# Optimization experiments

Hardware: AMD Instinct MI355X
Metric: run time of the kernel (lower is better)

## Reference

```python
import jax, jax.numpy as jnp
import numpy as np

EPS = 1e-5

def _rmsnorm(x, eps=1e-6):
    # non-affine RMSNorm over last dim (BitNet SubLN-style pre-quant norm)
    return x * jax.lax.rsqrt(jnp.mean(x * x, axis=-1, keepdims=True) + eps)

def _act_quant(x):
    # per-token int8 absmax quantization
    scale = 127.0 / jnp.clip(jnp.max(jnp.abs(x), axis=-1, keepdims=True), EPS)
    return jnp.clip(jnp.round(x * scale), -128, 127) / scale

def _weight_quant(w):
    # per-tensor ternary (1.58-bit) quantization
    scale = 1.0 / jnp.clip(jnp.mean(jnp.abs(w)), EPS)
    return jnp.clip(jnp.round(w * scale), -1, 1) / scale

def _ste(a, q):
    # straight-through estimator: forward = q, backward grad flows to a
    return a + jax.lax.stop_gradient(q - a)

def _bitlinear(x, w):
    # x: [..., in_features], w: [out_features, in_features], no bias
    xn = _rmsnorm(x)
    xq = _ste(xn, _act_quant(xn))
    wq = _ste(w, _weight_quant(w))
    return jnp.einsum('bsd,hd->bsh', xq, wq)


def setup_inputs() -> dict:
    key = jax.random.key(0)
    k_x, k1, k2, k3 = jax.random.split(key, 4)
    B, S, D, H = 4, 4096, 2048, 5632  # hidden = 256*ceil(2048*8/3 / 256)
    return {
        'x': jax.random.normal(k_x, (B, S, D), dtype=jnp.float32),
        'w1': jax.random.normal(k1, (H, D), dtype=jnp.float32) * 0.02,
        'w2': jax.random.normal(k2, (H, D), dtype=jnp.float32) * 0.02,
        'w3': jax.random.normal(k3, (D, H), dtype=jnp.float32) * 0.02,
    }


def reference(x, w1, w2, w3):
    gate = jax.nn.silu(_bitlinear(x, w1))
    up = _bitlinear(x, w2)
    return _bitlinear(gate * up, w3)
```

## Files before the change

kernel.cpp:

```cpp
#include <hip/hip_runtime.h>

typedef int i32x4 __attribute__((ext_vector_type(4)));

static constexpr int M_TOK = 16384;
static constexpr int D_IN  = 2048;
static constexpr int H_FF  = 5632;
static constexpr int NW    = H_FF * D_IN;

__device__ __forceinline__ void async16(const void* g, void* l) {
    __builtin_amdgcn_global_load_lds((__attribute__((address_space(1))) void*)g,
                                     (__attribute__((address_space(3))) void*)l,
                                     16, 0, 0);
}

__device__ __forceinline__ void sbar() {
    asm volatile("" ::: "memory");
    __builtin_amdgcn_s_barrier();
    asm volatile("" ::: "memory");
}
__device__ __forceinline__ void wait_lgkm0() {
    asm volatile("s_waitcnt lgkmcnt(0)" ::: "memory");
    __builtin_amdgcn_sched_barrier(0);
}

__global__ void absum_partial(const float4* __restrict__ w, int n4, double* __restrict__ part) {
    __shared__ double s[256];
    const int t = threadIdx.x;
    double acc = 0.0;
    for (int i = blockIdx.x * 256 + t; i < n4; i += gridDim.x * 256) {
        float4 v = w[i];
        acc += fabs((double)v.x) + fabs((double)v.y) + fabs((double)v.z) + fabs((double)v.w);
    }
    s[t] = acc;
    __syncthreads();
    for (int o = 128; o > 0; o >>= 1) {
        if (t < o) s[t] += s[t + o];
        __syncthreads();
    }
    if (t == 0) part[blockIdx.x] = s[0];
}

__global__ void finalize_scales(const double* __restrict__ parts, double* __restrict__ scales,
                                int nblocks, double inv_n) {
    const int t = threadIdx.x;
    if (t < 3) {
        const double* p = parts + t * nblocks;
        double s = 0.0;
        for (int i = 0; i < nblocks; ++i) s += p[i];
        double c = fmax(s * inv_n, 1e-5);
        scales[t * 2]     = 1.0 / c;
        scales[t * 2 + 1] = c;
    }
}

__global__ void quant_w_kernel(const float4* __restrict__ w, unsigned int* __restrict__ tw,
                               const double* __restrict__ scales, int idx, int n4) {
    const double s = scales[idx * 2];
    const int stride = gridDim.x * blockDim.x;
    for (int i = blockIdx.x * blockDim.x + threadIdx.x; i < n4; i += stride) {
        float4 v = w[i];
        int q0 = (int)fmin(fmax(rint((double)v.x * s), -1.0), 1.0);
        int q1 = (int)fmin(fmax(rint((double)v.y * s), -1.0), 1.0);
        int q2 = (int)fmin(fmax(rint((double)v.z * s), -1.0), 1.0);
        int q3 = (int)fmin(fmax(rint((double)v.w * s), -1.0), 1.0);
        tw[i] = (unsigned int)((q0 & 255) | ((q1 & 255) << 8) |
                               ((q2 & 255) << 16) | ((q3 & 255) << 24));
    }
}

__global__ void quant_x_kernel(const float* __restrict__ x, signed char* __restrict__ qx,
                               double* __restrict__ cx) {
    __shared__ double ssum[256];
    __shared__ float  smax[256];
    const int token = blockIdx.x;
    const int t = threadIdx.x;
    const float4* xr = (const float4*)(x + (size_t)token * D_IN);
    float4 v0 = xr[t];
    float4 v1 = xr[t + 256];
    double ss = (double)v0.x*v0.x + (double)v0.y*v0.y + (double)v0.z*v0.z + (double)v0.w*v0.w
              + (double)v1.x*v1.x + (double)v1.y*v1.y + (double)v1.z*v1.z + (double)v1.w*v1.w;
    float mx = fmaxf(fmaxf(fmaxf(fabsf(v0.x), fabsf(v0.y)), fmaxf(fabsf(v0.z), fabsf(v0.w))),
                     fmaxf(fmaxf(fabsf(v1.x), fabsf(v1.y)), fmaxf(fabsf(v1.z), fabsf(v1.w))));
    ssum[t] = ss; smax[t] = mx;
    __syncthreads();
    for (int o = 128; o > 0; o >>= 1) {
        if (t < o) { ssum[t] += ssum[t + o]; smax[t] = fmaxf(smax[t], smax[t + o]); }
        __syncthreads();
    }
    const double ms    = ssum[0] * (1.0 / (double)D_IN);
    const double r     = 1.0 / sqrt(ms + 1e-6);
    const double den   = fmax((double)smax[0] * r, 1e-5);
    const double scale = 127.0 / den;
    if (t == 0) cx[token] = den * (1.0 / 127.0);

    int q0 = (int)fmin(fmax(rint(((double)v0.x * r) * scale), -128.0), 127.0);
    int q1 = (int)fmin(fmax(rint(((double)v0.y * r) * scale), -128.0), 127.0);
    int q2 = (int)fmin(fmax(rint(((double)v0.z * r) * scale), -128.0), 127.0);
    int q3 = (int)fmin(fmax(rint(((double)v0.w * r) * scale), -128.0), 127.0);
    int q4 = (int)fmin(fmax(rint(((double)v1.x * r) * scale), -128.0), 127.0);
    int q5 = (int)fmin(fmax(rint(((double)v1.y * r) * scale), -128.0), 127.0);
    int q6 = (int)fmin(fmax(rint(((double)v1.z * r) * scale), -128.0), 127.0);
    int q7 = (int)fmin(fmax(rint(((double)v1.w * r) * scale), -128.0), 127.0);
    unsigned int* qr = (unsigned int*)(qx + (size_t)token * D_IN);
    qr[t]       = (unsigned int)((q0 & 255) | ((q1 & 255) << 8) | ((q2 & 255) << 16) | ((q3 & 255) << 24));
    qr[t + 256] = (unsigned int)((q4 & 255) | ((q5 & 255) << 8) | ((q6 & 255) << 16) | ((q7 & 255) << 24));
}

__global__ void quant_h_kernel(float* __restrict__ h, double* __restrict__ ch) {
    __shared__ double ssum[256];
    __shared__ float  smax[256];
    const int token = blockIdx.x;
    const int t = threadIdx.x;
    float* hr = h + (size_t)token * H_FF;
    float vals[22];
    double ss = 0.0;
    float mx = 0.f;
#pragma unroll
    for (int k = 0; k < 22; ++k) {
        float v = hr[t + 256 * k];
        vals[k] = v;
        ss += (double)v * (double)v;
        mx = fmaxf(mx, fabsf(v));
    }
    ssum[t] = ss; smax[t] = mx;
    __syncthreads();
    for (int o = 128; o > 0; o >>= 1) {
        if (t < o) { ssum[t] += ssum[t + o]; smax[t] = fmaxf(smax[t], smax[t + o]); }
        __syncthreads();
    }
    const double ms    = ssum[0] * (1.0 / (double)H_FF);
    const double r     = 1.0 / sqrt(ms + 1e-6);
    const double den   = fmax((double)smax[0] * r, 1e-5);
    const double scale = 127.0 / den;
    if (t == 0) ch[token] = den * (1.0 / 127.0);
    signed char* qr = (signed char*)hr;
#pragma unroll
    for (int k = 0; k < 22; ++k) {
        qr[t + 256 * k] =
            (signed char)(int)fmin(fmax(rint(((double)vals[k] * r) * scale), -128.0), 127.0);
    }
}

__global__ void __launch_bounds__(512, 2) gemm12_kernel(
    const signed char* __restrict__ qx,
    const signed char* __restrict__ tw1,
    const signed char* __restrict__ tw2,
    const double* __restrict__ cx,
    const double* __restrict__ scales,
    float* __restrict__ h)
{
    __shared__ __attribute__((aligned(16))) signed char lds[3][32768];

    const int t  = threadIdx.x;
    const int bn = blockIdx.x;
    const int bm = blockIdx.y;

    const int srow = t >> 2;
    const int scol = (t & 3) << 4;
    const signed char* gA  = qx  + (size_t)(bm * 256 + srow) * D_IN + scol;
    const signed char* gB1 = tw1 + (size_t)(bn * 128 + srow) * D_IN + scol;
    const signed char* gB2 = tw2 + (size_t)(bn * 128 + srow) * D_IN + scol;
    const size_t arstep = (size_t)128 * D_IN;
    const int l16 = t * 16;

    const int lane = t & 63;
    const int wv = t >> 6;
    const int wm = wv & 3;
    const int wn = wv >> 2;
    const int lm = lane & 15;
    const int kg = lane >> 4;

    int aoff[4], boff[4];
#pragma unroll
    for (int i = 0; i < 4; ++i) aoff[i] = (wm * 64 + i * 16 + lm) * 64 + kg * 16;
#pragma unroll
    for (int j = 0; j < 4; ++j) boff[j] = (wn * 64 + j * 16 + lm) * 64 + kg * 16;

    const i32x4 izero = {0, 0, 0, 0};
    i32x4 acc1[4][4], acc2[4][4];
#pragma unroll
    for (int i = 0; i < 4; ++i)
#pragma unroll
        for (int j = 0; j < 4; ++j) { acc1[i][j] = izero; acc2[i][j] = izero; }

    constexpr int NT = D_IN / 64;

#define STAGE_A12(buf, kt) { const int go = (kt) * 64;                       \
        async16(gA + go,          &lds[buf][l16]);                           \
        async16(gA + arstep + go, &lds[buf][l16 + 8192]); }
#define STAGE_B12(buf, kt) { const int go = (kt) * 64;                       \
        async16(gB1 + go, &lds[buf][16384 + l16]);                           \
        async16(gB2 + go, &lds[buf][24576 + l16]); }

    STAGE_A12(0, 0); STAGE_B12(0, 0);
    STAGE_A12(1, 1); STAGE_B12(1, 1);
    asm volatile("s_waitcnt vmcnt(4)" ::: "memory");
    sbar();

    for (int kt = 0; kt < NT; ++kt) {
        const int cur = kt % 3;
        const int nxt = (kt + 2) % 3;

        i32x4 a[4], b[4];
#pragma unroll
        for (int i = 0; i < 4; ++i) a[i] = *(const i32x4*)&lds[cur][aoff[i]];
#pragma unroll
        for (int j = 0; j < 4; ++j) b[j] = *(const i32x4*)&lds[cur][16384 + boff[j]];
        if (kt + 2 < NT) STAGE_A12(nxt, kt + 2);
        sbar();
        wait_lgkm0();
        __builtin_amdgcn_s_setprio(1);
#pragma unroll
        for (int i = 0; i < 4; ++i)
#pragma unroll
            for (int j = 0; j < 4; ++j)
                acc1[i][j] = __builtin_amdgcn_mfma_i32_16x16x64_i8(a[i], b[j], acc1[i][j], 0, 0, 0);
        __builtin_amdgcn_s_setprio(0);
        sbar();

#pragma unroll
        for (int j = 0; j < 4; ++j) b[j] = *(const i32x4*)&lds[cur][24576 + boff[j]];
        if (kt + 2 < NT) STAGE_B12(nxt, kt + 2);
        sbar();
        wait_lgkm0();
        __builtin_amdgcn_s_setprio(1);
#pragma unroll
        for (int i = 0; i < 4; ++i)
#pragma unroll
            for (int j = 0; j < 4; ++j)
                acc2[i][j] = __builtin_amdgcn_mfma_i32_16x16x64_i8(a[i], b[j], acc2[i][j], 0, 0, 0);
        __builtin_amdgcn_s_setprio(0);

        if (kt + 2 < NT)      { asm volatile("s_waitcnt vmcnt(4)" ::: "memory"); }
        else if (kt + 1 < NT) { asm volatile("s_waitcnt vmcnt(0)" ::: "memory"); }
        sbar();
    }
#undef STAGE_A12
#undef STAGE_B12

    const double cw1 = scales[1];
    const double cw2 = scales[3];
#pragma unroll
    for (int i = 0; i < 4; ++i) {
#pragma unroll
        for (int v = 0; v < 4; ++v) {
            const int row = bm * 256 + wm * 64 + i * 16 + kg * 4 + v;
            const double c  = cx[row];
            const double s1 = c * cw1, s2 = c * cw2;
            float* hp = h + (size_t)row * H_FF + bn * 128 + wn * 64 + lm;
#pragma unroll
            for (int j = 0; j < 4; ++j) {
                float g  = (float)((double)acc1[i][j][v] * s1);
                float u  = (float)((double)acc2[i][j][v] * s2);
                float sg = g / (1.0f + expf(-g));
                hp[j * 16] = sg * u;
            }
        }
    }
}

__global__ void __launch_bounds__(512, 2) gemm3_kernel(
    const signed char* __restrict__ qh,
    const signed char* __restrict__ tw3,
    const double* __restrict__ ch,
    const double* __restrict__ scales,
    float* __restrict__ out)
{
    __shared__ __attribute__((aligned(16))) signed char lds[3][32768];

    const int t  = threadIdx.x;
    const int bn = blockIdx.x;
    const int bm = blockIdx.y;

    const int srow = t >> 2;
    const int scol = (t & 3) << 4;
    const size_t qh_stride = (size_t)4 * H_FF;
    const signed char* gA = qh  + (size_t)(bm * 256 + srow) * qh_stride + scol;
    const signed char* gB = tw3 + (size_t)(bn * 256 + srow) * H_FF + scol;
    const size_t arstep = (size_t)128 * qh_stride;
    const size_t brstep = (size_t)128 * H_FF;
    const int l16 = t * 16;

    const int lane = t & 63;
    const int wv = t >> 6;
    const int wm = wv >> 2;
    const int wn = wv & 3;
    const int lm = lane & 15;
    const int kg = lane >> 4;

    int aoff[8], boff[4];
#pragma unroll
    for (int i = 0; i < 8; ++i) aoff[i] = (wm * 128 + i * 16 + lm) * 64 + kg * 16;
#pragma unroll
    for (int j = 0; j < 4; ++j) boff[j] = (wn * 64 + j * 16 + lm) * 64 + kg * 16;

    const i32x4 izero = {0, 0, 0, 0};
    i32x4 acc[8][4];
#pragma unroll
    for (int i = 0; i < 8; ++i)
#pragma unroll
        for (int j = 0; j < 4; ++j) acc[i][j] = izero;

    constexpr int NT = H_FF / 64;

#define STAGE_A3(buf, kt) { const int go = (kt) * 64;                        \
        async16(gA + go,          &lds[buf][l16]);                           \
        async16(gA + arstep + go, &lds[buf][l16 + 8192]); }
#define STAGE_B3(buf, kt) { const int go = (kt) * 64;                        \
        async16(gB + go,          &lds[buf][16384 + l16]);                   \
        async16(gB + brstep + go, &lds[buf][24576 + l16]); }

    STAGE_A3(0, 0); STAGE_B3(0, 0);
    STAGE_A3(1, 1); STAGE_B3(1, 1);
    asm volatile("s_waitcnt vmcnt(4)" ::: "memory");
    sbar();

    for (int kt = 0; kt < NT; ++kt) {
        const int cur = kt % 3;
        const int nxt = (kt + 2) % 3;

        i32x4 a[4], b[4], a2[4];
#pragma unroll
        for (int i = 0; i < 4; ++i) a[i] = *(const i32x4*)&lds[cur][aoff[i]];
#pragma unroll
        for (int j = 0; j < 4; ++j) b[j] = *(const i32x4*)&lds[cur][16384 + boff[j]];
        if (kt + 2 < NT) STAGE_A3(nxt, kt + 2);
        sbar();
        wait_lgkm0();
        __builtin_amdgcn_s_setprio(1);
#pragma unroll
        for (int i = 0; i < 4; ++i)
#pragma unroll
            for (int j = 0; j < 4; ++j)
                acc[i][j] = __builtin_amdgcn_mfma_i32_16x16x64_i8(a[i], b[j], acc[i][j], 0, 0, 0);
        __builtin_amdgcn_s_setprio(0);
        sbar();

#pragma unroll
        for (int i = 0; i < 4; ++i) a2[i] = *(const i32x4*)&lds[cur][aoff[i + 4]];
        if (kt + 2 < NT) STAGE_B3(nxt, kt + 2);
        sbar();
        wait_lgkm0();
        __builtin_amdgcn_s_setprio(1);
#pragma unroll
        for (int i = 0; i < 4; ++i)
#pragma unroll
            for (int j = 0; j < 4; ++j)
                acc[i + 4][j] = __builtin_amdgcn_mfma_i32_16x16x64_i8(a2[i], b[j], acc[i + 4][j], 0, 0, 0);
        __builtin_amdgcn_s_setprio(0);

        if (kt + 2 < NT)      { asm volatile("s_waitcnt vmcnt(4)" ::: "memory"); }
        else if (kt + 1 < NT) { asm volatile("s_waitcnt vmcnt(0)" ::: "memory"); }
        sbar();
    }
#undef STAGE_A3
#undef STAGE_B3

    const double cw3 = scales[5];
#pragma unroll
    for (int i = 0; i < 8; ++i) {
#pragma unroll
        for (int v = 0; v < 4; ++v) {
            const int row = bm * 256 + wm * 128 + i * 16 + kg * 4 + v;
            const double sc = ch[row] * cw3;
            float* op = out + (size_t)row * D_IN + bn * 256 + wn * 64 + lm;
#pragma unroll
            for (int j = 0; j < 4; ++j) op[j * 16] = (float)((double)acc[i][j][v] * sc);
        }
    }
}

extern "C" void kernel_launch(void* const* d_in, const int* in_sizes, int n_in,
                              void* d_out, int out_size, void* d_ws, size_t ws_size,
                              hipStream_t stream) {
    const float* x  = (const float*)d_in[0];
    const float* w1 = (const float*)d_in[1];
    const float* w2 = (const float*)d_in[2];
    const float* w3 = (const float*)d_in[3];

    char* ws = (char*)d_ws;
    double*      scales = (double*)(ws + 0);
    double*      parts  = (double*)(ws + 256);
    double*      cx     = (double*)(ws + 25088);
    double*      ch     = (double*)(ws + 156416);
    signed char* tw1    = (signed char*)(ws + 287744);
    signed char* tw2    = (signed char*)(ws + 11822336);
    signed char* tw3    = (signed char*)(ws + 23356928);
    float*       hb     = (float*)(ws + 34891520);
    signed char* qx     = (signed char*)(ws + 403990528);

    absum_partial<<<1024, 256, 0, stream>>>((const float4*)w1, NW / 4, parts);
    absum_partial<<<1024, 256, 0, stream>>>((const float4*)w2, NW / 4, parts + 1024);
    absum_partial<<<1024, 256, 0, stream>>>((const float4*)w3, NW / 4, parts + 2048);
    finalize_scales<<<1, 64, 0, stream>>>(parts, scales, 1024, 1.0 / (double)NW);
    quant_w_kernel<<<2048, 256, 0, stream>>>((const float4*)w1, (unsigned int*)tw1, scales, 0, NW / 4);
    quant_w_kernel<<<2048, 256, 0, stream>>>((const float4*)w2, (unsigned int*)tw2, scales, 1, NW / 4);
    quant_w_kernel<<<2048, 256, 0, stream>>>((const float4*)w3, (unsigned int*)tw3, scales, 2, NW / 4);
    quant_x_kernel<<<M_TOK, 256, 0, stream>>>(x, qx, cx);
    gemm12_kernel<<<dim3(H_FF / 128, M_TOK / 256), 512, 0, stream>>>(qx, tw1, tw2, cx, scales, hb);
    quant_h_kernel<<<M_TOK, 256, 0, stream>>>(hb, ch);
    gemm3_kernel<<<dim3(D_IN / 256, M_TOK / 256), 512, 0, stream>>>((const signed char*)hb,
                                                                    tw3, ch, scales,
                                                                    (float*)d_out);
}
```

Before: 1.114 ms.

## Swizzle LDS layout, remap block order for XCDs, vectorize h quantization

Both int8 GEMMs now XOR-swizzle the 16-byte column chunk when staging tiles into LDS and when reading MFMA fragments, to cut LDS bank conflicts. Both GEMMs also switch to a 1D grid with a remapped block index, so neighbouring blocks that run on the same XCD share A/B tiles in L2. The h quantization kernel now loads float2 and writes packed 16-bit pairs instead of single floats and bytes. The swizzle has to match exactly between the stage writes and the fragment reads, or results will be wrong.

```diff
diff --git a/kernel.cpp b/kernel.cpp
--- a/kernel.cpp
+++ b/kernel.cpp
@@ -112,15 +112,16 @@
     const int token = blockIdx.x;
     const int t = threadIdx.x;
     float* hr = h + (size_t)token * H_FF;
-    float vals[22];
+    const float2* h2 = (const float2*)hr;
+    float2 vals[11];
     double ss = 0.0;
     float mx = 0.f;
 #pragma unroll
-    for (int k = 0; k < 22; ++k) {
-        float v = hr[t + 256 * k];
+    for (int k = 0; k < 11; ++k) {
+        float2 v = h2[t + 256 * k];
         vals[k] = v;
-        ss += (double)v * (double)v;
-        mx = fmaxf(mx, fabsf(v));
+        ss += (double)v.x * (double)v.x + (double)v.y * (double)v.y;
+        mx = fmaxf(mx, fmaxf(fabsf(v.x), fabsf(v.y)));
     }
     ssum[t] = ss; smax[t] = mx;
     __syncthreads();
@@ -133,13 +134,15 @@
     const double den   = fmax((double)smax[0] * r, 1e-5);
     const double scale = 127.0 / den;
     if (t == 0) ch[token] = den * (1.0 / 127.0);
-    signed char* qr = (signed char*)hr;
-#pragma unroll
-    for (int k = 0; k < 22; ++k) {
-        qr[t + 256 * k] =
-            (signed char)(int)fmin(fmax(rint(((double)vals[k] * r) * scale), -128.0), 127.0);
-    }
-}
+    unsigned short* qr = (unsigned short*)hr;
+#pragma unroll
+    for (int k = 0; k < 11; ++k) {
+        int a = (int)fmin(fmax(rint(((double)vals[k].x * r) * scale), -128.0), 127.0);
+        int b = (int)fmin(fmax(rint(((double)vals[k].y * r) * scale), -128.0), 127.0);
+        qr[t + 256 * k] = (unsigned short)((a & 255) | ((b & 255) << 8));
+    }
+}
+
 
 __global__ void __launch_bounds__(512, 2) gemm12_kernel(
     const signed char* __restrict__ qx,
@@ -151,12 +154,13 @@
 {
     __shared__ __attribute__((aligned(16))) signed char lds[3][32768];
 
-    const int t  = threadIdx.x;
-    const int bn = blockIdx.x;
-    const int bm = blockIdx.y;
+    const int t = threadIdx.x;
+    const int swz = (blockIdx.x & 7) * 352 + (blockIdx.x >> 3);
+    const int bm  = swz & 63;
+    const int bn  = swz >> 6;
 
     const int srow = t >> 2;
-    const int scol = (t & 3) << 4;
+    const int scol = (((t & 3) ^ ((t >> 3) & 3)) << 4);
     const signed char* gA  = qx  + (size_t)(bm * 256 + srow) * D_IN + scol;
     const signed char* gB1 = tw1 + (size_t)(bn * 128 + srow) * D_IN + scol;
     const signed char* gB2 = tw2 + (size_t)(bn * 128 + srow) * D_IN + scol;
@@ -169,12 +173,13 @@
     const int wn = wv >> 2;
     const int lm = lane & 15;
     const int kg = lane >> 4;
+    const int koff = ((kg ^ ((lm >> 1) & 3)) << 4);
 
     int aoff[4], boff[4];
 #pragma unroll
-    for (int i = 0; i < 4; ++i) aoff[i] = (wm * 64 + i * 16 + lm) * 64 + kg * 16;
-#pragma unroll
-    for (int j = 0; j < 4; ++j) boff[j] = (wn * 64 + j * 16 + lm) * 64 + kg * 16;
+    for (int i = 0; i < 4; ++i) aoff[i] = (wm * 64 + i * 16 + lm) * 64 + koff;
+#pragma unroll
+    for (int j = 0; j < 4; ++j) boff[j] = (wn * 64 + j * 16 + lm) * 64 + koff;
 
     const i32x4 izero = {0, 0, 0, 0};
     i32x4 acc1[4][4], acc2[4][4];
@@ -268,12 +273,13 @@
 {
     __shared__ __attribute__((aligned(16))) signed char lds[3][32768];
 
-    const int t  = threadIdx.x;
-    const int bn = blockIdx.x;
-    const int bm = blockIdx.y;
+    const int t = threadIdx.x;
+    const int swz = (blockIdx.x & 7) * 64 + (blockIdx.x >> 3);
+    const int bm  = swz & 63;
+    const int bn  = swz >> 6;
 
     const int srow = t >> 2;
-    const int scol = (t & 3) << 4;
+    const int scol = (((t & 3) ^ ((t >> 3) & 3)) << 4);
     const size_t qh_stride = (size_t)4 * H_FF;
     const signed char* gA = qh  + (size_t)(bm * 256 + srow) * qh_stride + scol;
     const signed char* gB = tw3 + (size_t)(bn * 256 + srow) * H_FF + scol;
@@ -287,12 +293,13 @@
     const int wn = wv & 3;
     const int lm = lane & 15;
     const int kg = lane >> 4;
+    const int koff = ((kg ^ ((lm >> 1) & 3)) << 4);
 
     int aoff[8], boff[4];
 #pragma unroll
-    for (int i = 0; i < 8; ++i) aoff[i] = (wm * 128 + i * 16 + lm) * 64 + kg * 16;
-#pragma unroll
-    for (int j = 0; j < 4; ++j) boff[j] = (wn * 64 + j * 16 + lm) * 64 + kg * 16;
+    for (int i = 0; i < 8; ++i) aoff[i] = (wm * 128 + i * 16 + lm) * 64 + koff;
+#pragma unroll
+    for (int j = 0; j < 4; ++j) boff[j] = (wn * 64 + j * 16 + lm) * 64 + koff;
 
     const i32x4 izero = {0, 0, 0, 0};
     i32x4 acc[8][4];
@@ -397,9 +404,7 @@
     quant_w_kernel<<<2048, 256, 0, stream>>>((const float4*)w2, (unsigned int*)tw2, scales, 1, NW / 4);
     quant_w_kernel<<<2048, 256, 0, stream>>>((const float4*)w3, (unsigned int*)tw3, scales, 2, NW / 4);
     quant_x_kernel<<<M_TOK, 256, 0, stream>>>(x, qx, cx);
-    gemm12_kernel<<<dim3(H_FF / 128, M_TOK / 256), 512, 0, stream>>>(qx, tw1, tw2, cx, scales, hb);
+    gemm12_kernel<<<2816, 512, 0, stream>>>(qx, tw1, tw2, cx, scales, hb);
     quant_h_kernel<<<M_TOK, 256, 0, stream>>>(hb, ch);
-    gemm3_kernel<<<dim3(D_IN / 256, M_TOK / 256), 512, 0, stream>>>((const signed char*)hb,
-                                                                    tw3, ch, scales,
-                                                                    (float*)d_out);
-}
+    gemm3_kernel<<<512, 512, 0, stream>>>((const signed char*)hb, tw3, ch, scales, (float*)d_out);
+}
```

New measurement: 1.102 ms. About the same (-1.1%).
